# Optimization experiments

Hardware: AMD Instinct MI355X
Metric: run time of the kernel (lower is better)

Reference implementation:

```python
import jax, jax.numpy as jnp
import numpy as np

N_CLASSES = 16384
M = 2
D = 128


def setup_inputs() -> dict:
    key = jax.random.key(0)
    k1, k2 = jax.random.split(key)
    x = jax.random.normal(k1, (N_CLASSES * M, D), dtype=jnp.float32)
    anchor_idx = jax.random.randint(k2, (N_CLASSES,), 0, M, dtype=jnp.int64 if jax.config.jax_enable_x64 else jnp.int32).astype(jnp.int32)
    pos_idx = (1 - anchor_idx).astype(jnp.int32)  # randperm(2) -> positive is the other sample
    return {"x": x, "anchor_idx": anchor_idx, "pos_idx": pos_idx}


def reference(x, anchor_idx, pos_idx):
    # x: [N*M, D]; anchor_idx/pos_idx: [N] in [0, M)
    N = anchor_idx.shape[0]
    Dx = x.shape[1]
    xr = x.reshape(N, M, Dx)
    anchors = jnp.take_along_axis(xr, anchor_idx[:, None, None], axis=1)[:, 0, :]    # [N, D]
    positives = jnp.take_along_axis(xr, pos_idx[:, None, None], axis=1)[:, 0, :]     # [N, D]
    negs = xr[:, 1, :]                                                               # [N, D] (sample 1 of every class)
    # score[i, j] = a_i . (neg_j - pos_i) = a_i . neg_j - a_i . pos_i
    S = anchors @ negs.T                                                             # [N, N]
    ap = jnp.sum(anchors * positives, axis=1)                                        # [N]
    logits = S - ap[:, None]
    mask = ~jnp.eye(N, dtype=bool)                                                   # exclude j == i (own class)
    sums = jnp.sum(jnp.where(mask, jnp.exp(logits), jnp.float32(0.0)), axis=1)       # [N]
    return jnp.sum(jnp.log1p(sums))
```

## Files before the change

kernel.cpp:

```cpp
#include <hip/hip_runtime.h>
#include <hip/hip_bf16.h>
#include <math.h>

#define N_CLS 16384
#define DDIM  128
#define CSHIFT 50.0f
#define LOG2E 1.4426950408889634f
#define NEGC2 (-72.13475204444817f)

#if __has_builtin(__builtin_amdgcn_exp2f)
#define EXP2(x) __builtin_amdgcn_exp2f(x)
#else
#define EXP2(x) exp2f(x)
#endif

typedef __attribute__((ext_vector_type(8))) short short8;
typedef __attribute__((ext_vector_type(4))) float f32x4;

__device__ __forceinline__ unsigned short f2bf(float f) {
    __hip_bfloat16 h = __float2bfloat16(f);
    return *(unsigned short*)&h;
}

__global__ __launch_bounds__(256)
void prep_kernel(const float* __restrict__ x,
                 const int* __restrict__ aidx,
                 float* __restrict__ ap,
                 unsigned short* __restrict__ Afrag,
                 unsigned short* __restrict__ Bfrag,
                 float* __restrict__ out) {
    const int t = threadIdx.x;
    const int l = t & 31;
    const int i = blockIdx.x * 8 + (t >> 5);
    const float4 xa = *(const float4*)(x + (2L * i) * DDIM + l * 4);
    const float4 xb = *(const float4*)(x + (2L * i + 1) * DDIM + l * 4);
    const float4 av = (aidx[i] == 0) ? xa : xb;

    const int kc = l >> 3, q = (l >> 1) & 3, j0 = (l & 1) * 4;
    const long base = ((long)((i >> 4) * 4 + kc)) * 512 + (q * 16 + (i & 15)) * 8 + j0;

    ushort4 a4;
    a4.x = f2bf(av.x * LOG2E); a4.y = f2bf(av.y * LOG2E);
    a4.z = f2bf(av.z * LOG2E); a4.w = f2bf(av.w * LOG2E);
    *(ushort4*)(Afrag + base) = a4;

    ushort4 b4;
    b4.x = f2bf(xb.x); b4.y = f2bf(xb.y); b4.z = f2bf(xb.z); b4.w = f2bf(xb.w);
    *(ushort4*)(Bfrag + base) = b4;

    float d = xa.x * xb.x + xa.y * xb.y + xa.z * xb.z + xa.w * xb.w;
    d += __shfl_xor(d, 1, 64);
    d += __shfl_xor(d, 2, 64);
    d += __shfl_xor(d, 4, 64);
    d += __shfl_xor(d, 8, 64);
    d += __shfl_xor(d, 16, 64);
    if (l == 0) ap[i] = d;
    if (blockIdx.x == 0 && t == 0) out[0] = 0.0f;
}

__global__ __launch_bounds__(256, 2)
void fused_kernel(const unsigned short* __restrict__ Afrag,
                  const unsigned short* __restrict__ Bfrag,
                  float* __restrict__ partial) {
    const int tid = threadIdx.x;
    const int lane = tid & 63;
    const int w = tid >> 6;
    const int quad = lane >> 4;
    const int l15 = lane & 15;
    const int oct = blockIdx.x & 7;
    const int rt = blockIdx.x >> 3;
    const int wm2 = w >> 1;
    const int wh = w & 1;

    short8 af[4][4];
    {
        const unsigned short* abase =
            Afrag + ((long)(rt * 8 + wm2 * 4) * 4) * 512 + lane * 8;
        #pragma unroll
        for (int mt = 0; mt < 4; ++mt)
            #pragma unroll
            for (int kc = 0; kc < 4; ++kc)
                af[mt][kc] = *(const short8*)(abase + (mt * 4 + kc) * 512);
    }

    const unsigned short* bbase =
        Bfrag + ((long)(oct * 128 + wh * 4) * 4) * 512 + lane * 8;

    const f32x4 cinit = (f32x4){NEGC2, NEGC2, NEGC2, NEGC2};
    float rs[4][4] = {};
    short8 bP[4], bQ[4];
    f32x4 accA[4], accB[4];

    const bool canDiag = ((rt >> 4) == oct) && (wm2 == wh);
    const int itd = canDiag ? (rt & 15) : -1;

    auto mfma4 = [&](f32x4 (&acc)[4], short8 (&b)[4]) {
        #pragma unroll
        for (int mt = 0; mt < 4; ++mt)
            acc[mt] = __builtin_amdgcn_mfma_f32_16x16x32_bf16(
                af[mt][0], b[0], cinit, 0, 0, 0);
        #pragma unroll
        for (int kc = 1; kc < 4; ++kc)
            #pragma unroll
            for (int mt = 0; mt < 4; ++mt)
                acc[mt] = __builtin_amdgcn_mfma_f32_16x16x32_bf16(
                    af[mt][kc], b[kc], acc[mt], 0, 0, 0);
    };
    auto epi = [&](f32x4 (&acc)[4]) {
        #pragma unroll
        for (int mt = 0; mt < 4; ++mt)
            #pragma unroll
            for (int reg = 0; reg < 4; ++reg)
                rs[mt][reg] += EXP2(acc[mt][reg]);
    };
    auto epiD = [&](f32x4 (&acc)[4], int nt) {
        #pragma unroll
        for (int mt = 0; mt < 4; ++mt)
            #pragma unroll
            for (int reg = 0; reg < 4; ++reg) {
                float e = EXP2(acc[mt][reg]);
                if (mt == nt) e = (quad * 4 + reg == l15) ? 0.0f : e;
                rs[mt][reg] += e;
            }
    };

    #pragma unroll
    for (int kc = 0; kc < 4; ++kc)
        bP[kc] = *(const short8*)(bbase + kc * 512);

    bool dprev = false;
    for (int it = 0; it < 16; ++it) {
        const unsigned short* p1 = bbase + (long)it * 16384;
        const bool d = (it == itd);

        #pragma unroll
        for (int kc = 0; kc < 4; ++kc)
            bQ[kc] = *(const short8*)(p1 + 2048 + kc * 512);
        mfma4(accA, bP);
        if (it > 0) { if (dprev) epiD(accB, 3); else epi(accB); }

        #pragma unroll
        for (int kc = 0; kc < 4; ++kc)
            bP[kc] = *(const short8*)(p1 + 4096 + kc * 512);
        mfma4(accB, bQ);
        if (d) epiD(accA, 0); else epi(accA);

        #pragma unroll
        for (int kc = 0; kc < 4; ++kc)
            bQ[kc] = *(const short8*)(p1 + 6144 + kc * 512);
        mfma4(accA, bP);
        if (d) epiD(accB, 1); else epi(accB);

        const unsigned short* p2 = bbase + (long)((it < 15) ? it + 1 : it) * 16384;
        #pragma unroll
        for (int kc = 0; kc < 4; ++kc)
            bP[kc] = *(const short8*)(p2 + kc * 512);
        mfma4(accB, bQ);
        if (d) epiD(accA, 2); else epi(accA);

        dprev = d;
    }
    if (dprev) epiD(accB, 3); else epi(accB);

    const int slot = oct * 2 + wh;
    const int rowBase = rt * 128 + wm2 * 64;
    #pragma unroll
    for (int mt = 0; mt < 4; ++mt)
        #pragma unroll
        for (int reg = 0; reg < 4; ++reg) {
            float v = rs[mt][reg];
            v += __shfl_xor(v, 1, 64);
            v += __shfl_xor(v, 2, 64);
            v += __shfl_xor(v, 4, 64);
            v += __shfl_xor(v, 8, 64);
            if (l15 == 0)
                partial[(long)slot * N_CLS + rowBase + mt * 16 + quad * 4 + reg] = v;
        }
}

__global__ __launch_bounds__(256)
void finalize_kernel(const float* __restrict__ partial,
                     const float* __restrict__ ap,
                     float* __restrict__ out) {
    __shared__ float red[256];
    const int t = threadIdx.x;
    const int row = blockIdx.x * 256 + t;
    float s = 0.0f;
    #pragma unroll
    for (int p = 0; p < 16; ++p) s += partial[(long)p * N_CLS + row];
    const float u = logf(s) + (CSHIFT - ap[row]);
    const float loss = (u > 25.0f) ? u : log1pf(__expf(u));
    red[t] = loss;
    __syncthreads();
    for (int st = 128; st > 0; st >>= 1) {
        if (t < st) red[t] += red[t + st];
        __syncthreads();
    }
    if (t == 0) atomicAdd(out, red[0]);
}

extern "C" void kernel_launch(void* const* d_in, const int* in_sizes, int n_in,
                              void* d_out, int out_size, void* d_ws, size_t ws_size,
                              hipStream_t stream) {
    const float* x    = (const float*)d_in[0];
    const int*   aidx = (const int*)d_in[1];

    char* ws = (char*)d_ws;
    float* ap             = (float*)(ws);
    float* partial        = (float*)(ws + 131072);
    unsigned short* Afrag = (unsigned short*)(ws + 131072 + 1048576);
    unsigned short* Bfrag = (unsigned short*)(ws + 131072 + 1048576 + 4194304);

    prep_kernel<<<N_CLS / 8, 256, 0, stream>>>(x, aidx, ap, Afrag, Bfrag, (float*)d_out);
    fused_kernel<<<1024, 256, 0, stream>>>(Afrag, Bfrag, partial);
    finalize_kernel<<<64, 256, 0, stream>>>(partial, ap, (float*)d_out);
}
```

Before: 139.0 us.

## Retile fused kernel to 32-row warp tiles over full column range, raise occupancy

Each wave now owns 32 anchor rows (2 M-tiles) and sweeps all 1024 columns of its column octant, instead of 64 rows over half the columns. This halves the register footprint of A fragments and accumulators so launch bounds can go from 2 to 4 blocks per SIMD, and partial sums drop from 16 slots to 8. The prep kernel is also rewritten to emit full 16-byte fragment stores and reduce the anchor-positive dot via shared memory. The trade-off is that each B fragment is reused across fewer MFMAs, so more B global loads are issued per unit of math.

```diff
diff --git a/kernel.cpp b/kernel.cpp
--- a/kernel.cpp
+++ b/kernel.cpp
@@ -30,35 +30,40 @@
                  unsigned short* __restrict__ Bfrag,
                  float* __restrict__ out) {
     const int t = threadIdx.x;
-    const int l = t & 31;
-    const int i = blockIdx.x * 8 + (t >> 5);
-    const float4 xa = *(const float4*)(x + (2L * i) * DDIM + l * 4);
-    const float4 xb = *(const float4*)(x + (2L * i + 1) * DDIM + l * 4);
-    const float4 av = (aidx[i] == 0) ? xa : xb;
-
-    const int kc = l >> 3, q = (l >> 1) & 3, j0 = (l & 1) * 4;
-    const long base = ((long)((i >> 4) * 4 + kc)) * 512 + (q * 16 + (i & 15)) * 8 + j0;
-
-    ushort4 a4;
-    a4.x = f2bf(av.x * LOG2E); a4.y = f2bf(av.y * LOG2E);
-    a4.z = f2bf(av.z * LOG2E); a4.w = f2bf(av.w * LOG2E);
-    *(ushort4*)(Afrag + base) = a4;
-
-    ushort4 b4;
-    b4.x = f2bf(xb.x); b4.y = f2bf(xb.y); b4.z = f2bf(xb.z); b4.w = f2bf(xb.w);
-    *(ushort4*)(Bfrag + base) = b4;
-
-    float d = xa.x * xb.x + xa.y * xb.y + xa.z * xb.z + xa.w * xb.w;
-    d += __shfl_xor(d, 1, 64);
-    d += __shfl_xor(d, 2, 64);
-    d += __shfl_xor(d, 4, 64);
-    d += __shfl_xor(d, 8, 64);
+    const int tl = blockIdx.x;
+    const int kc = t >> 6, q = (t >> 4) & 3, m = t & 15;
+    const int col = kc * 32 + q * 8;
+    const int i = tl * 16 + m;
+
+    float fa[8], fb[8];
+    *(float4*)&fa[0] = *(const float4*)(x + (2L * i) * DDIM + col);
+    *(float4*)&fa[4] = *(const float4*)(x + (2L * i) * DDIM + col + 4);
+    *(float4*)&fb[0] = *(const float4*)(x + (2L * i + 1) * DDIM + col);
+    *(float4*)&fb[4] = *(const float4*)(x + (2L * i + 1) * DDIM + col + 4);
+    const bool sel = (aidx[i] != 0);
+
+    short8 As8, Bs8;
+    float d = 0.0f;
+    #pragma unroll
+    for (int j = 0; j < 8; ++j) {
+        const float av = sel ? fb[j] : fa[j];
+        As8[j] = (short)f2bf(av * LOG2E);
+        Bs8[j] = (short)f2bf(fb[j]);
+        d += fa[j] * fb[j];
+    }
+    *(short8*)(Afrag + (long)tl * 2048 + t * 8) = As8;
+    *(short8*)(Bfrag + (long)tl * 2048 + t * 8) = Bs8;
+
     d += __shfl_xor(d, 16, 64);
-    if (l == 0) ap[i] = d;
-    if (blockIdx.x == 0 && t == 0) out[0] = 0.0f;
-}
-
-__global__ __launch_bounds__(256, 2)
+    d += __shfl_xor(d, 32, 64);
+    __shared__ float sap[4][16];
+    if ((t & 63) < 16) sap[kc][t & 63] = d;
+    __syncthreads();
+    if (t < 16) ap[tl * 16 + t] = sap[0][t] + sap[1][t] + sap[2][t] + sap[3][t];
+    if (t == 0 && tl == 0) out[0] = 0.0f;
+}
+
+__global__ __launch_bounds__(256, 4)
 void fused_kernel(const unsigned short* __restrict__ Afrag,
                   const unsigned short* __restrict__ Bfrag,
                   float* __restrict__ partial) {
@@ -69,103 +74,91 @@
     const int l15 = lane & 15;
     const int oct = blockIdx.x & 7;
     const int rt = blockIdx.x >> 3;
-    const int wm2 = w >> 1;
-    const int wh = w & 1;
-
-    short8 af[4][4];
+
+    short8 af[2][4];
     {
         const unsigned short* abase =
-            Afrag + ((long)(rt * 8 + wm2 * 4) * 4) * 512 + lane * 8;
-        #pragma unroll
-        for (int mt = 0; mt < 4; ++mt)
+            Afrag + ((long)(rt * 8 + w * 2) * 4) * 512 + lane * 8;
+        #pragma unroll
+        for (int mt = 0; mt < 2; ++mt)
             #pragma unroll
             for (int kc = 0; kc < 4; ++kc)
                 af[mt][kc] = *(const short8*)(abase + (mt * 4 + kc) * 512);
     }
 
-    const unsigned short* bbase =
-        Bfrag + ((long)(oct * 128 + wh * 4) * 4) * 512 + lane * 8;
+    const unsigned short* bbase = Bfrag + (long)oct * 262144 + lane * 8;
 
     const f32x4 cinit = (f32x4){NEGC2, NEGC2, NEGC2, NEGC2};
-    float rs[4][4] = {};
-    short8 bP[4], bQ[4];
-    f32x4 accA[4], accB[4];
-
-    const bool canDiag = ((rt >> 4) == oct) && (wm2 == wh);
-    const int itd = canDiag ? (rt & 15) : -1;
-
-    auto mfma4 = [&](f32x4 (&acc)[4], short8 (&b)[4]) {
-        #pragma unroll
-        for (int mt = 0; mt < 4; ++mt)
-            acc[mt] = __builtin_amdgcn_mfma_f32_16x16x32_bf16(
-                af[mt][0], b[0], cinit, 0, 0, 0);
-        #pragma unroll
-        for (int kc = 1; kc < 4; ++kc)
-            #pragma unroll
-            for (int mt = 0; mt < 4; ++mt)
-                acc[mt] = __builtin_amdgcn_mfma_f32_16x16x32_bf16(
-                    af[mt][kc], b[kc], acc[mt], 0, 0, 0);
+    float rs[2][4] = {};
+    short8 b[2][4];
+    f32x4 acc[2][2];
+
+    const bool canD = ((rt >> 4) == oct);
+    const int itd = rt & 15;
+    auto mtdOf = [&](bool dd, int nt2) -> int {
+        const int md = nt2 - 2 * w;
+        return (dd && (md == 0 || md == 1)) ? md : -1;
     };
-    auto epi = [&](f32x4 (&acc)[4]) {
-        #pragma unroll
-        for (int mt = 0; mt < 4; ++mt)
+    auto epi = [&](f32x4 (&a)[2]) {
+        #pragma unroll
+        for (int mt = 0; mt < 2; ++mt)
             #pragma unroll
             for (int reg = 0; reg < 4; ++reg)
-                rs[mt][reg] += EXP2(acc[mt][reg]);
+                rs[mt][reg] += EXP2(a[mt][reg]);
     };
-    auto epiD = [&](f32x4 (&acc)[4], int nt) {
-        #pragma unroll
-        for (int mt = 0; mt < 4; ++mt)
+    auto epiD = [&](f32x4 (&a)[2], int mtd) {
+        #pragma unroll
+        for (int mt = 0; mt < 2; ++mt)
             #pragma unroll
             for (int reg = 0; reg < 4; ++reg) {
-                float e = EXP2(acc[mt][reg]);
-                if (mt == nt) e = (quad * 4 + reg == l15) ? 0.0f : e;
+                float e = EXP2(a[mt][reg]);
+                if (mt == mtd && quad * 4 + reg == l15) e = 0.0f;
                 rs[mt][reg] += e;
             }
     };
 
     #pragma unroll
     for (int kc = 0; kc < 4; ++kc)
-        bP[kc] = *(const short8*)(bbase + kc * 512);
+        b[0][kc] = *(const short8*)(bbase + kc * 512);
 
     bool dprev = false;
     for (int it = 0; it < 16; ++it) {
-        const unsigned short* p1 = bbase + (long)it * 16384;
-        const bool d = (it == itd);
-
-        #pragma unroll
-        for (int kc = 0; kc < 4; ++kc)
-            bQ[kc] = *(const short8*)(p1 + 2048 + kc * 512);
-        mfma4(accA, bP);
-        if (it > 0) { if (dprev) epiD(accB, 3); else epi(accB); }
-
-        #pragma unroll
-        for (int kc = 0; kc < 4; ++kc)
-            bP[kc] = *(const short8*)(p1 + 4096 + kc * 512);
-        mfma4(accB, bQ);
-        if (d) epiD(accA, 0); else epi(accA);
-
-        #pragma unroll
-        for (int kc = 0; kc < 4; ++kc)
-            bQ[kc] = *(const short8*)(p1 + 6144 + kc * 512);
-        mfma4(accA, bP);
-        if (d) epiD(accB, 1); else epi(accB);
-
-        const unsigned short* p2 = bbase + (long)((it < 15) ? it + 1 : it) * 16384;
-        #pragma unroll
-        for (int kc = 0; kc < 4; ++kc)
-            bP[kc] = *(const short8*)(p2 + kc * 512);
-        mfma4(accB, bQ);
-        if (d) epiD(accA, 2); else epi(accA);
-
+        const bool d = canD && (it == itd);
+        const long itoff = (long)it * 16384;
+        #pragma unroll
+        for (int nt = 0; nt < 8; ++nt) {
+            const int cb = nt & 1, ob = cb ^ 1;
+            const long nxt = (it == 15 && nt == 7) ? itoff + nt * 2048
+                                                   : itoff + nt * 2048 + 2048;
+            #pragma unroll
+            for (int kc = 0; kc < 4; ++kc)
+                b[ob][kc] = *(const short8*)(bbase + nxt + kc * 512);
+            acc[cb][0] = __builtin_amdgcn_mfma_f32_16x16x32_bf16(
+                af[0][0], b[cb][0], cinit, 0, 0, 0);
+            acc[cb][1] = __builtin_amdgcn_mfma_f32_16x16x32_bf16(
+                af[1][0], b[cb][0], cinit, 0, 0, 0);
+            #pragma unroll
+            for (int kc = 1; kc < 4; ++kc) {
+                acc[cb][0] = __builtin_amdgcn_mfma_f32_16x16x32_bf16(
+                    af[0][kc], b[cb][kc], acc[cb][0], 0, 0, 0);
+                acc[cb][1] = __builtin_amdgcn_mfma_f32_16x16x32_bf16(
+                    af[1][kc], b[cb][kc], acc[cb][1], 0, 0, 0);
+            }
+            if (it > 0 || nt > 0) {
+                const int mtd = (nt == 0) ? mtdOf(dprev, 7) : mtdOf(d, nt - 1);
+                if (mtd < 0) epi(acc[ob]); else epiD(acc[ob], mtd);
+            }
+        }
         dprev = d;
     }
-    if (dprev) epiD(accB, 3); else epi(accB);
-
-    const int slot = oct * 2 + wh;
-    const int rowBase = rt * 128 + wm2 * 64;
-    #pragma unroll
-    for (int mt = 0; mt < 4; ++mt)
+    {
+        const int mtd = mtdOf(dprev, 7);
+        if (mtd < 0) epi(acc[1]); else epiD(acc[1], mtd);
+    }
+
+    const int rowBase = rt * 128 + w * 32;
+    #pragma unroll
+    for (int mt = 0; mt < 2; ++mt)
         #pragma unroll
         for (int reg = 0; reg < 4; ++reg) {
             float v = rs[mt][reg];
@@ -174,7 +167,7 @@
             v += __shfl_xor(v, 4, 64);
             v += __shfl_xor(v, 8, 64);
             if (l15 == 0)
-                partial[(long)slot * N_CLS + rowBase + mt * 16 + quad * 4 + reg] = v;
+                partial[(long)oct * N_CLS + rowBase + mt * 16 + quad * 4 + reg] = v;
         }
 }
 
@@ -187,7 +180,7 @@
     const int row = blockIdx.x * 256 + t;
     float s = 0.0f;
     #pragma unroll
-    for (int p = 0; p < 16; ++p) s += partial[(long)p * N_CLS + row];
+    for (int p = 0; p < 8; ++p) s += partial[(long)p * N_CLS + row];
     const float u = logf(s) + (CSHIFT - ap[row]);
     const float loss = (u > 25.0f) ? u : log1pf(__expf(u));
     red[t] = loss;
@@ -211,7 +204,7 @@
     unsigned short* Afrag = (unsigned short*)(ws + 131072 + 1048576);
     unsigned short* Bfrag = (unsigned short*)(ws + 131072 + 1048576 + 4194304);
 
-    prep_kernel<<<N_CLS / 8, 256, 0, stream>>>(x, aidx, ap, Afrag, Bfrag, (float*)d_out);
+    prep_kernel<<<N_CLS / 16, 256, 0, stream>>>(x, aidx, ap, Afrag, Bfrag, (float*)d_out);
     fused_kernel<<<1024, 256, 0, stream>>>(Afrag, Bfrag, partial);
     finalize_kernel<<<64, 256, 0, stream>>>(partial, ap, (float*)d_out);
 }
```

Result: slower. 221.8 us (+59.6%).
